# Performance work log

Measured on AMD Instinct MI355X. Metric: run time of the kernel, lower is better.

Reference implementation:

```python
import jax, jax.numpy as jnp
import numpy as np

WS = 8          # window size
NH = 16         # num heads
C = 256         # in_channels
L = WS * WS     # tokens per window
EPS = 1e-5      # LayerNorm eps

def _rel_index():
    coords = np.stack(np.meshgrid(np.arange(WS), np.arange(WS), indexing='ij')).reshape(2, -1)
    rel = coords[:, :, None] - coords[:, None, :]
    rel = rel + (WS - 1)
    rel[0] = rel[0] * (2 * WS - 1)
    return jnp.asarray(rel.sum(0))  # [L, L] int

REL_IDX = _rel_index()

def _ln(x, g, b):
    m = x.mean(-1, keepdims=True)
    v = jnp.var(x, axis=-1, keepdims=True)
    return (x - m) * jax.lax.rsqrt(v + EPS) * g + b

def setup_inputs() -> dict:
    key = jax.random.key(0)
    ks = jax.random.split(key, 8)
    return {
        'x': jax.random.normal(ks[0], (2, C, 256, 256), dtype=jnp.float32),
        'pre_gamma': jnp.ones((C,), jnp.float32),
        'pre_beta': jnp.zeros((C,), jnp.float32),
        'post_gamma': jnp.ones((C,), jnp.float32),
        'post_beta': jnp.zeros((C,), jnp.float32),
        'qkv_w': jax.random.normal(ks[1], (C, 3 * C), jnp.float32) * 0.02,
        'qkv_b': jnp.zeros((3 * C,), jnp.float32),
        'proj_w': jax.random.normal(ks[2], (C, C), jnp.float32) * 0.02,
        'proj_b': jnp.zeros((C,), jnp.float32),
        'rel_bias_table': jax.random.normal(ks[3], ((2 * WS - 1) ** 2, NH), jnp.float32) * 0.02,
    }

def reference(x, pre_gamma, pre_beta, post_gamma, post_beta, qkv_w, qkv_b, proj_w, proj_b, rel_bias_table):
    N, Cc, H, W = x.shape
    # block partition: [N,C,H,W] -> [N*nWin, L, C]
    t = x.reshape(N, Cc, H // WS, WS, W // WS, WS)
    t = t.transpose(0, 2, 4, 3, 5, 1).reshape(-1, L, Cc)
    B = t.shape[0]
    # pre-norm + relative self-attention (cosine / normalized qk)
    y = _ln(t, pre_gamma, pre_beta)
    qkv = (y @ qkv_w + qkv_b).reshape(B, L, 3, NH, Cc // NH).transpose(2, 0, 3, 1, 4)
    q, k, v = qkv[0], qkv[1], qkv[2]  # [B, h, L, dh]
    q = q / jnp.maximum(jnp.linalg.norm(q, axis=-1, keepdims=True), 1e-12)
    k = k / jnp.maximum(jnp.linalg.norm(k, axis=-1, keepdims=True), 1e-12)
    bias = rel_bias_table[REL_IDX].transpose(2, 0, 1)  # [h, L, L]
    attn = jax.nn.softmax(jnp.einsum('bhld,bhmd->bhlm', q, k) + bias, axis=-1)
    o = jnp.einsum('bhlm,bhmd->bhld', attn, v).transpose(0, 2, 1, 3).reshape(B, L, Cc)
    o = o @ proj_w + proj_b
    out = t + o
    # post-norm residual (mlp is Identity in MetNet-3)
    out = out + _ln(out, post_gamma, post_beta)
    # reverse partition -> [N, C, H, W]
    out = out.reshape(N, H // WS, W // WS, WS, WS, Cc)
    out = out.transpose(0, 5, 1, 3, 2, 4).reshape(N, Cc, H, W)
    return out
```

## Files before the change

kernel.cpp:

```cpp
#include <hip/hip_runtime.h>


#define WSZ 8
#define LTOK 64
#define NH 16
#define CCH 256
#define WW2 256
#define HWP 65536
#define NWIN 2048

#define TP 258
#define QP2 18
#define VP2 66
#define PP2 66
#define OHP 36

typedef __bf16 bf16x8 __attribute__((ext_vector_type(8)));
typedef float  f32x4  __attribute__((ext_vector_type(4)));
typedef unsigned short u16;
typedef uint4  __attribute__((may_alias)) uint4_a;
typedef float4 __attribute__((may_alias)) float4_a;

__device__ __forceinline__ float b2f(u16 u) {
    return (float)__builtin_bit_cast(__bf16, u);
}
__device__ __forceinline__ u16 f2b(float f) {
    return __builtin_bit_cast(u16, (__bf16)f);
}
__device__ __forceinline__ __bf16 u2b(u16 u) {
    return __builtin_bit_cast(__bf16, u);
}
__device__ __forceinline__ float gload(const void* p, int idx, int isf32) {
    return isf32 ? ((const float*)p)[idx] : b2f(((const u16*)p)[idx]);
}

static __global__ void detect_dtype(const u16* __restrict__ xu, int* __restrict__ flag) {
    int lane = threadIdx.x;
    u16 u = xu[lane];
    int e = (u >> 7) & 0xFF;
    bool plaus = (u == 0) || (e >= 0x6C && e <= 0x86);
    unsigned long long m = __ballot(plaus);
    if (lane == 0) flag[0] = (__popcll(m) >= 56) ? 0 : 1;
}

static __global__ __launch_bounds__(256) void prep_qkv(
        const void* __restrict__ qkv_w, const void* __restrict__ qkv_b,
        const void* __restrict__ g, const void* __restrict__ be,
        u16* __restrict__ gwT, float* __restrict__ D2, float* __restrict__ D3,
        const int* __restrict__ flagp)
{
    const int isf32 = flagp[0];
    int col = blockIdx.x;
    int c   = threadIdx.x;
    float gv = gload(g, c, isf32), bv = gload(be, c, isf32);
    float wv = gload(qkv_w, c * 768 + col, isf32);
    gwT[col * 256 + c] = f2b(gv * wv);
    float s2 = gv * wv, s3 = bv * wv;
    #pragma unroll
    for (int off = 32; off; off >>= 1) {
        s2 += __shfl_xor(s2, off);
        s3 += __shfl_xor(s3, off);
    }
    __shared__ float p2[4], p3[4];
    int wvid = threadIdx.x >> 6, ln = threadIdx.x & 63;
    if (ln == 0) { p2[wvid] = s2; p3[wvid] = s3; }
    __syncthreads();
    if (threadIdx.x == 0) {
        D2[col] = p2[0] + p2[1] + p2[2] + p2[3];
        D3[col] = p3[0] + p3[1] + p3[2] + p3[3] + gload(qkv_b, col, isf32);
    }
}

static __global__ __launch_bounds__(256) void prep_proj(
        const void* __restrict__ proj_w, u16* __restrict__ pwT,
        const void* __restrict__ table, float* __restrict__ tablef,
        const int* __restrict__ flagp)
{
    const int isf32 = flagp[0];
    int nrow = blockIdx.x, k = threadIdx.x;
    pwT[nrow * 256 + k] = f2b(gload(proj_w, k * 256 + nrow, isf32));
    int gid = blockIdx.x * 256 + threadIdx.x;
    if (gid < (2 * WSZ - 1) * (2 * WSZ - 1) * NH)
        tablef[gid] = gload(table, gid, isf32);
}

static __global__ __launch_bounds__(256, 3) void win_attn(
    const void* __restrict__ x, void* __restrict__ out,
    const u16* __restrict__ gwT, const u16* __restrict__ pwT,
    const float* __restrict__ D2, const float* __restrict__ D3,
    const void* __restrict__ proj_b, const void* __restrict__ postg,
    const void* __restrict__ postb, const float* __restrict__ tablef,
    const int* __restrict__ flagp)
{
    __shared__ u16 sm_t[LTOK * TP];
    __shared__ u16 sm_q[LTOK * QP2];
    __shared__ u16 sm_k[LTOK * QP2];
    __shared__ u16 sm_vt[NH * VP2];
    __shared__ u16 sm_p[LTOK * PP2];
    __shared__ u16 sm_oh[LTOK * OHP];
    __shared__ float sm_mean[LTOK], sm_rstd[LTOK];
    __shared__ u16 sm_zero[16];

    const int isf32 = flagp[0];
    const int tid  = threadIdx.x;
    const int wv   = tid >> 6;
    const int lane = tid & 63;
    const int quad = lane >> 4;
    const int n15  = lane & 15;

    const int b  = blockIdx.x;
    const int nb = b >> 10, wh = (b >> 5) & 31, wwi = b & 31;
    const int base = nb * (CCH * HWP) + wh * (8 * WW2) + wwi * 8;

    if (tid < 16) sm_zero[tid] = 0;

    if (isf32) {
        const float* xf = (const float*)x;
        #pragma unroll
        for (int r = 0; r < 8; ++r) {
            int s = tid + r * 256;
            int c = s >> 3, i = s & 7;
            const float* src = xf + base + c * HWP + i * WW2;
            float4 a = *(const float4_a*)(src);
            float4 d = *(const float4_a*)(src + 4);
            u16* dst = &sm_t[(i * 8) * TP + c];
            dst[0 * TP] = f2b(a.x);  dst[1 * TP] = f2b(a.y);
            dst[2 * TP] = f2b(a.z);  dst[3 * TP] = f2b(a.w);
            dst[4 * TP] = f2b(d.x);  dst[5 * TP] = f2b(d.y);
            dst[6 * TP] = f2b(d.z);  dst[7 * TP] = f2b(d.w);
        }
    } else {
        const u16* xu = (const u16*)x;
        #pragma unroll
        for (int r = 0; r < 8; ++r) {
            int s = tid + r * 256;
            int c = s >> 3, i = s & 7;
            const uint4 v = *(const uint4_a*)(xu + base + c * HWP + i * WW2);
            u16* dst = &sm_t[(i * 8) * TP + c];
            dst[0 * TP] = (u16)(v.x & 0xffff);  dst[1 * TP] = (u16)(v.x >> 16);
            dst[2 * TP] = (u16)(v.y & 0xffff);  dst[3 * TP] = (u16)(v.y >> 16);
            dst[4 * TP] = (u16)(v.z & 0xffff);  dst[5 * TP] = (u16)(v.z >> 16);
            dst[6 * TP] = (u16)(v.w & 0xffff);  dst[7 * TP] = (u16)(v.w >> 16);
        }
    }
    __syncthreads();

    {
        int l = tid >> 2, g = tid & 3;
        float s = 0.f, ss = 0.f;
        const u16* row = &sm_t[l * TP + g * 64];
        #pragma unroll
        for (int e = 0; e < 64; ++e) {
            float a = b2f(row[e]);
            s += a; ss += a * a;
        }
        s += __shfl_xor(s, 1); ss += __shfl_xor(ss, 1);
        s += __shfl_xor(s, 2); ss += __shfl_xor(ss, 2);
        if (g == 0) {
            float mean = s * (1.f / 256.f);
            float var  = ss * (1.f / 256.f) - mean * mean;
            sm_mean[l] = mean;
            sm_rstd[l] = rsqrtf(var + 1e-5f);
        }
    }

    float s4[4], ms4[4];
    #pragma unroll
    for (int r = 0; r < 4; ++r) {
        int tok = wv * 16 + quad * 4 + r;
        float mu = sm_mean[tok], sd = sm_rstd[tok];
        s4[r] = sd; ms4[r] = -mu * sd;
    }

    bf16x8 afr[8];
    {
        const u16* arow = &sm_t[(wv * 16 + n15) * TP];
        #pragma unroll
        for (int kb = 0; kb < 8; ++kb) {
            #pragma unroll
            for (int j = 0; j < 8; ++j)
                afr[kb][j] = u2b(arow[kb * 32 + quad * 8 + j]);
        }
    }

    int toff[4][4];
    #pragma unroll
    for (int ct = 0; ct < 4; ++ct) {
        int key = ct * 16 + n15, im = key >> 3, jm = key & 7;
        #pragma unroll
        for (int r = 0; r < 4; ++r) {
            int tok = wv * 16 + quad * 4 + r;
            int il = tok >> 3, jl = tok & 7;
            toff[ct][r] = ((il - im + 7) * 15 + (jl - jm + 7)) * 16;
        }
    }

    f32x4 accp[16];
    #pragma unroll
    for (int t2 = 0; t2 < 16; ++t2) accp[t2] = f32x4{0.f, 0.f, 0.f, 0.f};
    const f32x4 zero4 = f32x4{0.f, 0.f, 0.f, 0.f};

    for (int h = 0; h < 16; ++h) {
        f32x4 aq = zero4, ak = zero4, av = zero4;
        const u16* gq = &gwT[(h * 16 + n15) * 256 + quad * 8];
        const u16* gk = gq + 256 * 256;
        const u16* gv = gq + 512 * 256;
        #pragma unroll
        for (int kb = 0; kb < 8; ++kb) {
            bf16x8 bq = __builtin_bit_cast(bf16x8, *(const uint4_a*)(gq + kb * 32));
            bf16x8 bk = __builtin_bit_cast(bf16x8, *(const uint4_a*)(gk + kb * 32));
            bf16x8 bv = __builtin_bit_cast(bf16x8, *(const uint4_a*)(gv + kb * 32));
            aq = __builtin_amdgcn_mfma_f32_16x16x32_bf16(afr[kb], bq, aq, 0, 0, 0);
            ak = __builtin_amdgcn_mfma_f32_16x16x32_bf16(afr[kb], bk, ak, 0, 0, 0);
            av = __builtin_amdgcn_mfma_f32_16x16x32_bf16(afr[kb], bv, av, 0, 0, 0);
        }
        float d2q = D2[h * 16 + n15],       d3q = D3[h * 16 + n15];
        float d2k = D2[256 + h * 16 + n15], d3k = D3[256 + h * 16 + n15];
        float d2v = D2[512 + h * 16 + n15], d3v = D3[512 + h * 16 + n15];
        float qv[4], kv[4], vv[4];
        #pragma unroll
        for (int r = 0; r < 4; ++r) {
            qv[r] = s4[r] * aq[r] + ms4[r] * d2q + d3q;
            kv[r] = s4[r] * ak[r] + ms4[r] * d2k + d3k;
            vv[r] = s4[r] * av[r] + ms4[r] * d2v + d3v;
        }
        #pragma unroll
        for (int r = 0; r < 4; ++r) {
            float sq = qv[r] * qv[r], sk = kv[r] * kv[r];
            sq += __shfl_xor(sq, 1); sk += __shfl_xor(sk, 1);
            sq += __shfl_xor(sq, 2); sk += __shfl_xor(sk, 2);
            sq += __shfl_xor(sq, 4); sk += __shfl_xor(sk, 4);
            sq += __shfl_xor(sq, 8); sk += __shfl_xor(sk, 8);
            qv[r] *= rsqrtf(fmaxf(sq, 1e-24f));
            kv[r] *= rsqrtf(fmaxf(sk, 1e-24f));
        }
        #pragma unroll
        for (int r = 0; r < 4; ++r) {
            int tok = wv * 16 + quad * 4 + r;
            sm_q[tok * QP2 + n15] = f2b(qv[r]);
            sm_k[tok * QP2 + n15] = f2b(kv[r]);
            sm_vt[n15 * VP2 + tok] = f2b(vv[r]);
        }
        __syncthreads();

        f32x4 sc[4];
        {
            bf16x8 aqf;
            const u16* qrow = (quad < 2) ? &sm_q[(wv * 16 + n15) * QP2 + quad * 8]
                                         : sm_zero;
            #pragma unroll
            for (int j = 0; j < 8; ++j) aqf[j] = u2b(qrow[j]);
            #pragma unroll
            for (int ct = 0; ct < 4; ++ct) {
                bf16x8 bkf;
                const u16* krow = (quad < 2) ? &sm_k[(ct * 16 + n15) * QP2 + quad * 8]
                                             : sm_zero;
                #pragma unroll
                for (int j = 0; j < 8; ++j) bkf[j] = u2b(krow[j]);
                f32x4 bias;
                #pragma unroll
                for (int r = 0; r < 4; ++r) bias[r] = tablef[toff[ct][r] + h];
                sc[ct] = __builtin_amdgcn_mfma_f32_16x16x32_bf16(aqf, bkf, bias, 0, 0, 0);
            }
        }
        float inv[4];
        #pragma unroll
        for (int r = 0; r < 4; ++r) {
            float e0 = __expf(sc[0][r]), e1 = __expf(sc[1][r]);
            float e2 = __expf(sc[2][r]), e3 = __expf(sc[3][r]);
            int tok = wv * 16 + quad * 4 + r;
            sm_p[tok * PP2 +  0 + n15] = f2b(e0);
            sm_p[tok * PP2 + 16 + n15] = f2b(e1);
            sm_p[tok * PP2 + 32 + n15] = f2b(e2);
            sm_p[tok * PP2 + 48 + n15] = f2b(e3);
            float sm = (e0 + e1) + (e2 + e3);
            sm += __shfl_xor(sm, 1); sm += __shfl_xor(sm, 2);
            sm += __shfl_xor(sm, 4); sm += __shfl_xor(sm, 8);
            inv[r] = 1.f / sm;
        }

        f32x4 ov = zero4;
        #pragma unroll
        for (int ks = 0; ks < 2; ++ks) {
            bf16x8 ap, bvf;
            const u16* prow = &sm_p[(wv * 16 + n15) * PP2 + ks * 32 + quad * 8];
            const u16* vrow = &sm_vt[n15 * VP2 + ks * 32 + quad * 8];
            #pragma unroll
            for (int j = 0; j < 8; ++j) { ap[j] = u2b(prow[j]); bvf[j] = u2b(vrow[j]); }
            ov = __builtin_amdgcn_mfma_f32_16x16x32_bf16(ap, bvf, ov, 0, 0, 0);
        }
        #pragma unroll
        for (int r = 0; r < 4; ++r) {
            int tok = wv * 16 + quad * 4 + r;
            sm_oh[tok * OHP + (h & 1) * 16 + n15] = f2b(ov[r] * inv[r]);
        }

        if (h & 1) {
            int hp = h >> 1;
            bf16x8 aof;
            const u16* orow = &sm_oh[(wv * 16 + n15) * OHP + quad * 8];
            #pragma unroll
            for (int j = 0; j < 8; ++j) aof[j] = u2b(orow[j]);
            const u16* pwb = &pwT[n15 * 256 + hp * 32 + quad * 8];
            #pragma unroll
            for (int t2 = 0; t2 < 16; ++t2) {
                bf16x8 bpf = __builtin_bit_cast(bf16x8, *(const uint4_a*)(pwb + t2 * 16 * 256));
                accp[t2] = __builtin_amdgcn_mfma_f32_16x16x32_bf16(aof, bpf, accp[t2], 0, 0, 0);
            }
        }
        __syncthreads();
    }

    {
        #pragma unroll
        for (int t2 = 0; t2 < 16; ++t2) {
            int col = t2 * 16 + n15;
            float pb = gload(proj_b, col, isf32);
            #pragma unroll
            for (int r = 0; r < 4; ++r) {
                int tok = wv * 16 + quad * 4 + r;
                accp[t2][r] += pb + b2f(sm_t[tok * TP + col]);
            }
        }
        float sr[4] = {0, 0, 0, 0}, ssr[4] = {0, 0, 0, 0};
        #pragma unroll
        for (int t2 = 0; t2 < 16; ++t2) {
            #pragma unroll
            for (int r = 0; r < 4; ++r) { float v = accp[t2][r]; sr[r] += v; ssr[r] += v * v; }
        }
        #pragma unroll
        for (int r = 0; r < 4; ++r) {
            sr[r] += __shfl_xor(sr[r], 1); ssr[r] += __shfl_xor(ssr[r], 1);
            sr[r] += __shfl_xor(sr[r], 2); ssr[r] += __shfl_xor(ssr[r], 2);
            sr[r] += __shfl_xor(sr[r], 4); ssr[r] += __shfl_xor(ssr[r], 4);
            sr[r] += __shfl_xor(sr[r], 8); ssr[r] += __shfl_xor(ssr[r], 8);
        }
        float mean2[4], rs2[4];
        #pragma unroll
        for (int r = 0; r < 4; ++r) {
            float m = sr[r] * (1.f / 256.f);
            float v = ssr[r] * (1.f / 256.f) - m * m;
            mean2[r] = m; rs2[r] = rsqrtf(v + 1e-5f);
        }
        #pragma unroll
        for (int t2 = 0; t2 < 16; ++t2) {
            int col = t2 * 16 + n15;
            float pg = gload(postg, col, isf32), pb2 = gload(postb, col, isf32);
            #pragma unroll
            for (int r = 0; r < 4; ++r) {
                int tok = wv * 16 + quad * 4 + r;
                float o1 = accp[t2][r];
                float fin = o1 + (o1 - mean2[r]) * rs2[r] * pg + pb2;
                sm_t[tok * TP + col] = f2b(fin);
            }
        }
    }
    __syncthreads();

    if (isf32) {
        float* outf = (float*)out;
        #pragma unroll
        for (int r = 0; r < 8; ++r) {
            int s = tid + r * 256;
            int c = s >> 3, i = s & 7;
            const u16* src = &sm_t[(i * 8) * TP + c];
            float* dst = outf + base + c * HWP + i * WW2;
            float4 a, d;
            a.x = b2f(src[0 * TP]); a.y = b2f(src[1 * TP]);
            a.z = b2f(src[2 * TP]); a.w = b2f(src[3 * TP]);
            d.x = b2f(src[4 * TP]); d.y = b2f(src[5 * TP]);
            d.z = b2f(src[6 * TP]); d.w = b2f(src[7 * TP]);
            *(float4_a*)dst = a;
            *(float4_a*)(dst + 4) = d;
        }
    } else {
        u16* outu = (u16*)out;
        #pragma unroll
        for (int r = 0; r < 8; ++r) {
            int s = tid + r * 256;
            int c = s >> 3, i = s & 7;
            const u16* src = &sm_t[(i * 8) * TP + c];
            uint4 v;
            v.x = (unsigned)src[0 * TP] | ((unsigned)src[1 * TP] << 16);
            v.y = (unsigned)src[2 * TP] | ((unsigned)src[3 * TP] << 16);
            v.z = (unsigned)src[4 * TP] | ((unsigned)src[5 * TP] << 16);
            v.w = (unsigned)src[6 * TP] | ((unsigned)src[7 * TP] << 16);
            *(uint4_a*)(outu + base + c * HWP + i * WW2) = v;
        }
    }
}

extern "C" void kernel_launch(void* const* d_in, const int* in_sizes, int n_in,
                              void* d_out, int out_size, void* d_ws, size_t ws_size,
                              hipStream_t stream) {
    const void* x     = d_in[0];
    const void* preg  = d_in[1];
    const void* preb  = d_in[2];
    const void* postg = d_in[3];
    const void* postb = d_in[4];
    const void* qkvw  = d_in[5];
    const void* qkvb  = d_in[6];
    const void* projw = d_in[7];
    const void* projb = d_in[8];
    const void* table = d_in[9];

    char* ws = (char*)d_ws;
    u16*   gwT = (u16*)(ws);
    u16*   pwT = (u16*)(ws + 393216);
    float* D2  = (float*)(ws + 524288);
    float* D3  = (float*)(ws + 527360);
    float* tbf = (float*)(ws + 530432);
    int*   flg = (int*)(ws + 544832);

    detect_dtype<<<1, 64, 0, stream>>>((const u16*)x, flg);
    prep_qkv<<<768, 256, 0, stream>>>(qkvw, qkvb, preg, preb, gwT, D2, D3, flg);
    prep_proj<<<256, 256, 0, stream>>>(projw, pwT, table, tbf, flg);
    win_attn<<<NWIN, 256, 0, stream>>>(x, d_out, gwT, pwT, D2, D3,
                                       projb, postg, postb, tbf, flg);
}
```

Before: 1.064 ms.

## Batch QKV projection over four heads and compute softmax row sums via MFMA

Restructures the per-head loop into groups of four heads: QKV projections for four heads are computed together, with per-head shared buffers for q, k and v^T, so only one pair of block barriers is needed per group instead of per head. The softmax denominator is now computed with an extra MFMA against a ones vector, replacing the shuffle reduction. It also lowers the occupancy hint from 3 to 2 blocks per CU to allow the larger accumulator register set. The tradeoffs are more shared memory and registers, fewer resident blocks, and row sums taken over the bf16-rounded probabilities.

```diff
diff --git a/kernel.cpp b/kernel.cpp
--- a/kernel.cpp
+++ b/kernel.cpp
@@ -84,7 +84,7 @@
         tablef[gid] = gload(table, gid, isf32);
 }
 
-static __global__ __launch_bounds__(256, 3) void win_attn(
+static __global__ __launch_bounds__(256, 2) void win_attn(
     const void* __restrict__ x, void* __restrict__ out,
     const u16* __restrict__ gwT, const u16* __restrict__ pwT,
     const float* __restrict__ D2, const float* __restrict__ D3,
@@ -93,9 +93,9 @@
     const int* __restrict__ flagp)
 {
     __shared__ u16 sm_t[LTOK * TP];
-    __shared__ u16 sm_q[LTOK * QP2];
-    __shared__ u16 sm_k[LTOK * QP2];
-    __shared__ u16 sm_vt[NH * VP2];
+    __shared__ u16 sm_q[4][LTOK * QP2];
+    __shared__ u16 sm_k[4][LTOK * QP2];
+    __shared__ u16 sm_vt[4][NH * VP2];
     __shared__ u16 sm_p[LTOK * PP2];
     __shared__ u16 sm_oh[LTOK * OHP];
     __shared__ float sm_mean[LTOK], sm_rstd[LTOK];
@@ -200,112 +200,126 @@
     for (int t2 = 0; t2 < 16; ++t2) accp[t2] = f32x4{0.f, 0.f, 0.f, 0.f};
     const f32x4 zero4 = f32x4{0.f, 0.f, 0.f, 0.f};
 
-    for (int h = 0; h < 16; ++h) {
-        f32x4 aq = zero4, ak = zero4, av = zero4;
-        const u16* gq = &gwT[(h * 16 + n15) * 256 + quad * 8];
-        const u16* gk = gq + 256 * 256;
-        const u16* gv = gq + 512 * 256;
+    bf16x8 onesf;
+    #pragma unroll
+    for (int j = 0; j < 8; ++j) onesf[j] = (__bf16)1.0f;
+
+    for (int hq = 0; hq < 4; ++hq) {
+        const int H = hq * 4;
+
+        f32x4 aq[4], ak[4], av[4];
+        #pragma unroll
+        for (int hh = 0; hh < 4; ++hh) { aq[hh] = zero4; ak[hh] = zero4; av[hh] = zero4; }
+        const u16* g0 = &gwT[(H * 16 + n15) * 256 + quad * 8];
         #pragma unroll
         for (int kb = 0; kb < 8; ++kb) {
-            bf16x8 bq = __builtin_bit_cast(bf16x8, *(const uint4_a*)(gq + kb * 32));
-            bf16x8 bk = __builtin_bit_cast(bf16x8, *(const uint4_a*)(gk + kb * 32));
-            bf16x8 bv = __builtin_bit_cast(bf16x8, *(const uint4_a*)(gv + kb * 32));
-            aq = __builtin_amdgcn_mfma_f32_16x16x32_bf16(afr[kb], bq, aq, 0, 0, 0);
-            ak = __builtin_amdgcn_mfma_f32_16x16x32_bf16(afr[kb], bk, ak, 0, 0, 0);
-            av = __builtin_amdgcn_mfma_f32_16x16x32_bf16(afr[kb], bv, av, 0, 0, 0);
-        }
-        float d2q = D2[h * 16 + n15],       d3q = D3[h * 16 + n15];
-        float d2k = D2[256 + h * 16 + n15], d3k = D3[256 + h * 16 + n15];
-        float d2v = D2[512 + h * 16 + n15], d3v = D3[512 + h * 16 + n15];
-        float qv[4], kv[4], vv[4];
-        #pragma unroll
-        for (int r = 0; r < 4; ++r) {
-            qv[r] = s4[r] * aq[r] + ms4[r] * d2q + d3q;
-            kv[r] = s4[r] * ak[r] + ms4[r] * d2k + d3k;
-            vv[r] = s4[r] * av[r] + ms4[r] * d2v + d3v;
-        }
-        #pragma unroll
-        for (int r = 0; r < 4; ++r) {
-            float sq = qv[r] * qv[r], sk = kv[r] * kv[r];
-            sq += __shfl_xor(sq, 1); sk += __shfl_xor(sk, 1);
-            sq += __shfl_xor(sq, 2); sk += __shfl_xor(sk, 2);
-            sq += __shfl_xor(sq, 4); sk += __shfl_xor(sk, 4);
-            sq += __shfl_xor(sq, 8); sk += __shfl_xor(sk, 8);
-            qv[r] *= rsqrtf(fmaxf(sq, 1e-24f));
-            kv[r] *= rsqrtf(fmaxf(sk, 1e-24f));
-        }
-        #pragma unroll
-        for (int r = 0; r < 4; ++r) {
-            int tok = wv * 16 + quad * 4 + r;
-            sm_q[tok * QP2 + n15] = f2b(qv[r]);
-            sm_k[tok * QP2 + n15] = f2b(kv[r]);
-            sm_vt[n15 * VP2 + tok] = f2b(vv[r]);
+            #pragma unroll
+            for (int hh = 0; hh < 4; ++hh) {
+                const u16* gq = g0 + hh * 4096 + kb * 32;
+                bf16x8 bq = __builtin_bit_cast(bf16x8, *(const uint4_a*)(gq));
+                bf16x8 bk = __builtin_bit_cast(bf16x8, *(const uint4_a*)(gq + 65536));
+                bf16x8 bv = __builtin_bit_cast(bf16x8, *(const uint4_a*)(gq + 131072));
+                aq[hh] = __builtin_amdgcn_mfma_f32_16x16x32_bf16(afr[kb], bq, aq[hh], 0, 0, 0);
+                ak[hh] = __builtin_amdgcn_mfma_f32_16x16x32_bf16(afr[kb], bk, ak[hh], 0, 0, 0);
+                av[hh] = __builtin_amdgcn_mfma_f32_16x16x32_bf16(afr[kb], bv, av[hh], 0, 0, 0);
+            }
+        }
+        #pragma unroll
+        for (int hh = 0; hh < 4; ++hh) {
+            int ci = (H + hh) * 16 + n15;
+            float d2q = D2[ci],       d3q = D3[ci];
+            float d2k = D2[256 + ci], d3k = D3[256 + ci];
+            float d2v = D2[512 + ci], d3v = D3[512 + ci];
+            float qv[4], kv[4], vv[4];
+            #pragma unroll
+            for (int r = 0; r < 4; ++r) {
+                qv[r] = s4[r] * aq[hh][r] + ms4[r] * d2q + d3q;
+                kv[r] = s4[r] * ak[hh][r] + ms4[r] * d2k + d3k;
+                vv[r] = s4[r] * av[hh][r] + ms4[r] * d2v + d3v;
+            }
+            #pragma unroll
+            for (int r = 0; r < 4; ++r) {
+                float sq = qv[r] * qv[r], sk = kv[r] * kv[r];
+                sq += __shfl_xor(sq, 1); sk += __shfl_xor(sk, 1);
+                sq += __shfl_xor(sq, 2); sk += __shfl_xor(sk, 2);
+                sq += __shfl_xor(sq, 4); sk += __shfl_xor(sk, 4);
+                sq += __shfl_xor(sq, 8); sk += __shfl_xor(sk, 8);
+                qv[r] *= rsqrtf(fmaxf(sq, 1e-24f));
+                kv[r] *= rsqrtf(fmaxf(sk, 1e-24f));
+            }
+            #pragma unroll
+            for (int r = 0; r < 4; ++r) {
+                int tok = wv * 16 + quad * 4 + r;
+                sm_q[hh][tok * QP2 + n15] = f2b(qv[r]);
+                sm_k[hh][tok * QP2 + n15] = f2b(kv[r]);
+                sm_vt[hh][n15 * VP2 + tok] = f2b(vv[r]);
+            }
         }
         __syncthreads();
 
-        f32x4 sc[4];
-        {
-            bf16x8 aqf;
-            const u16* qrow = (quad < 2) ? &sm_q[(wv * 16 + n15) * QP2 + quad * 8]
-                                         : sm_zero;
-            #pragma unroll
-            for (int j = 0; j < 8; ++j) aqf[j] = u2b(qrow[j]);
-            #pragma unroll
-            for (int ct = 0; ct < 4; ++ct) {
-                bf16x8 bkf;
-                const u16* krow = (quad < 2) ? &sm_k[(ct * 16 + n15) * QP2 + quad * 8]
+        #pragma unroll
+        for (int hh = 0; hh < 4; ++hh) {
+            const int h = H + hh;
+            f32x4 sc[4];
+            {
+                bf16x8 aqf;
+                const u16* qrow = (quad < 2) ? &sm_q[hh][(wv * 16 + n15) * QP2 + quad * 8]
                                              : sm_zero;
                 #pragma unroll
-                for (int j = 0; j < 8; ++j) bkf[j] = u2b(krow[j]);
-                f32x4 bias;
+                for (int j = 0; j < 8; ++j) aqf[j] = u2b(qrow[j]);
                 #pragma unroll
-                for (int r = 0; r < 4; ++r) bias[r] = tablef[toff[ct][r] + h];
-                sc[ct] = __builtin_amdgcn_mfma_f32_16x16x32_bf16(aqf, bkf, bias, 0, 0, 0);
-            }
-        }
-        float inv[4];
-        #pragma unroll
-        for (int r = 0; r < 4; ++r) {
-            float e0 = __expf(sc[0][r]), e1 = __expf(sc[1][r]);
-            float e2 = __expf(sc[2][r]), e3 = __expf(sc[3][r]);
-            int tok = wv * 16 + quad * 4 + r;
-            sm_p[tok * PP2 +  0 + n15] = f2b(e0);
-            sm_p[tok * PP2 + 16 + n15] = f2b(e1);
-            sm_p[tok * PP2 + 32 + n15] = f2b(e2);
-            sm_p[tok * PP2 + 48 + n15] = f2b(e3);
-            float sm = (e0 + e1) + (e2 + e3);
-            sm += __shfl_xor(sm, 1); sm += __shfl_xor(sm, 2);
-            sm += __shfl_xor(sm, 4); sm += __shfl_xor(sm, 8);
-            inv[r] = 1.f / sm;
-        }
-
-        f32x4 ov = zero4;
-        #pragma unroll
-        for (int ks = 0; ks < 2; ++ks) {
-            bf16x8 ap, bvf;
-            const u16* prow = &sm_p[(wv * 16 + n15) * PP2 + ks * 32 + quad * 8];
-            const u16* vrow = &sm_vt[n15 * VP2 + ks * 32 + quad * 8];
-            #pragma unroll
-            for (int j = 0; j < 8; ++j) { ap[j] = u2b(prow[j]); bvf[j] = u2b(vrow[j]); }
-            ov = __builtin_amdgcn_mfma_f32_16x16x32_bf16(ap, bvf, ov, 0, 0, 0);
-        }
-        #pragma unroll
-        for (int r = 0; r < 4; ++r) {
-            int tok = wv * 16 + quad * 4 + r;
-            sm_oh[tok * OHP + (h & 1) * 16 + n15] = f2b(ov[r] * inv[r]);
-        }
-
-        if (h & 1) {
-            int hp = h >> 1;
-            bf16x8 aof;
-            const u16* orow = &sm_oh[(wv * 16 + n15) * OHP + quad * 8];
-            #pragma unroll
-            for (int j = 0; j < 8; ++j) aof[j] = u2b(orow[j]);
-            const u16* pwb = &pwT[n15 * 256 + hp * 32 + quad * 8];
-            #pragma unroll
-            for (int t2 = 0; t2 < 16; ++t2) {
-                bf16x8 bpf = __builtin_bit_cast(bf16x8, *(const uint4_a*)(pwb + t2 * 16 * 256));
-                accp[t2] = __builtin_amdgcn_mfma_f32_16x16x32_bf16(aof, bpf, accp[t2], 0, 0, 0);
+                for (int ct = 0; ct < 4; ++ct) {
+                    bf16x8 bkf;
+                    const u16* krow = (quad < 2) ? &sm_k[hh][(ct * 16 + n15) * QP2 + quad * 8]
+                                                 : sm_zero;
+                    #pragma unroll
+                    for (int j = 0; j < 8; ++j) bkf[j] = u2b(krow[j]);
+                    f32x4 bias;
+                    #pragma unroll
+                    for (int r = 0; r < 4; ++r) bias[r] = tablef[toff[ct][r] + h];
+                    sc[ct] = __builtin_amdgcn_mfma_f32_16x16x32_bf16(aqf, bkf, bias, 0, 0, 0);
+                }
+            }
+            #pragma unroll
+            for (int r = 0; r < 4; ++r) {
+                float e0 = __expf(sc[0][r]), e1 = __expf(sc[1][r]);
+                float e2 = __expf(sc[2][r]), e3 = __expf(sc[3][r]);
+                int tok = wv * 16 + quad * 4 + r;
+                sm_p[tok * PP2 +  0 + n15] = f2b(e0);
+                sm_p[tok * PP2 + 16 + n15] = f2b(e1);
+                sm_p[tok * PP2 + 32 + n15] = f2b(e2);
+                sm_p[tok * PP2 + 48 + n15] = f2b(e3);
+            }
+
+            f32x4 ov = zero4, rs = zero4;
+            #pragma unroll
+            for (int ks = 0; ks < 2; ++ks) {
+                bf16x8 ap, bvf;
+                const u16* prow = &sm_p[(wv * 16 + n15) * PP2 + ks * 32 + quad * 8];
+                const u16* vrow = &sm_vt[hh][n15 * VP2 + ks * 32 + quad * 8];
+                #pragma unroll
+                for (int j = 0; j < 8; ++j) { ap[j] = u2b(prow[j]); bvf[j] = u2b(vrow[j]); }
+                ov = __builtin_amdgcn_mfma_f32_16x16x32_bf16(ap, bvf, ov, 0, 0, 0);
+                rs = __builtin_amdgcn_mfma_f32_16x16x32_bf16(ap, onesf, rs, 0, 0, 0);
+            }
+            #pragma unroll
+            for (int r = 0; r < 4; ++r) {
+                int tok = wv * 16 + quad * 4 + r;
+                sm_oh[tok * OHP + (h & 1) * 16 + n15] = f2b(ov[r] / rs[r]);
+            }
+
+            if (hh & 1) {
+                int hp = h >> 1;
+                bf16x8 aof;
+                const u16* orow = &sm_oh[(wv * 16 + n15) * OHP + quad * 8];
+                #pragma unroll
+                for (int j = 0; j < 8; ++j) aof[j] = u2b(orow[j]);
+                const u16* pwb = &pwT[n15 * 256 + hp * 32 + quad * 8];
+                #pragma unroll
+                for (int t2 = 0; t2 < 16; ++t2) {
+                    bf16x8 bpf = __builtin_bit_cast(bf16x8, *(const uint4_a*)(pwb + t2 * 16 * 256));
+                    accp[t2] = __builtin_amdgcn_mfma_f32_16x16x32_bf16(aof, bpf, accp[t2], 0, 0, 0);
+                }
             }
         }
         __syncthreads();
```

New measurement: 976.3 us. 8.3% less time.
